# Optimization experiments

Measured on AMD Instinct MI355X. Metric: run time of the kernel, lower is better.

The kernel has to match this reference:

```python
import jax, jax.numpy as jnp
import numpy as np

T, B, C, H = 1024, 4, 1024, 16
NH = C // H  # head_size = 64
E = 32       # TIME_MIX_EXTRA_DIM


def setup_inputs():
    key = jax.random.key(0)
    ks = jax.random.split(key, 12)
    scale = 1.0 / np.sqrt(C)

    def time_p(ratio):
        w = jnp.arange(C, dtype=jnp.float32) / C
        return (1.0 - jnp.power(w, ratio))[None, None, :]

    decay_speed = jnp.array([-6.0 + 5.0 * (h / (C - 1)) ** 0.7 for h in range(C)], jnp.float32)
    tfa = jnp.array([0.1 * ((i + 1) % 3 - 1) for i in range(C)], jnp.float32).reshape(H, NH)
    return dict(
        inputs=jax.random.normal(ks[0], (T, B, C), jnp.float32),
        shifted=jax.random.normal(ks[1], (B, C), jnp.float32),
        state=jnp.zeros((B, H, NH, NH), jnp.float32),
        time_maa_x=time_p(1.0), time_maa_w=time_p(1.0), time_maa_k=time_p(1.0),
        time_maa_v=time_p(1.0), time_maa_r=time_p(0.5), time_maa_g=time_p(0.5),
        time_maa_w1=jax.random.uniform(ks[2], (C, E * 5), jnp.float32, -1e-4, 1e-4),
        time_maa_w2=jax.random.uniform(ks[3], (5, E, C), jnp.float32, -1e-4, 1e-4),
        Wr=jax.random.normal(ks[4], (C, C), jnp.float32) * scale,
        Wk=jax.random.normal(ks[5], (C, C), jnp.float32) * scale,
        Wv=jax.random.normal(ks[6], (C, C), jnp.float32) * scale,
        Wg=jax.random.normal(ks[7], (C, C), jnp.float32) * scale,
        Wo=jax.random.normal(ks[8], (C, C), jnp.float32) * scale,
        time_decay_w1=jax.random.uniform(ks[9], (C, E), jnp.float32, -1e-4, 1e-4),
        time_decay_w2=jax.random.uniform(ks[10], (E, C), jnp.float32, -1e-4, 1e-4),
        time_decay=decay_speed[None, None, :],
        time_faaaa=tfa,
        gn_scale=jnp.ones((C,), jnp.float32) + 0.02 * jax.random.normal(ks[11], (C,), jnp.float32),
        gn_bias=jnp.zeros((C,), jnp.float32),
    )


def _wkv(r, k, v, w, tf, state):
    # r,k,v,w: (T,B,H,N); tf: (H,N,1); state: (B,H,N,N)
    def body(st, inp):
        rt, kt, vt, wt = inp
        a = kt[..., :, None] * vt[..., None, :]              # (B,H,N,N) outer product
        out = jnp.einsum('bhn,bhnm->bhm', rt, tf * a + st)   # (B,H,N)
        st = a + wt[..., None] * st
        return st, out
    state, out = jax.lax.scan(body, state, (r, k, v, w))
    return out, state


def reference(inputs, shifted, state, time_maa_x, time_maa_w, time_maa_k,
              time_maa_v, time_maa_r, time_maa_g, time_maa_w1, time_maa_w2,
              Wr, Wk, Wv, Wg, Wo, time_decay_w1, time_decay_w2, time_decay,
              time_faaaa, gn_scale, gn_bias):
    Tl, Bl, Cl = inputs.shape
    Hh, Nh = time_faaaa.shape
    x = inputs
    prev = jnp.concatenate([shifted[None], inputs[:-1]], axis=0)  # token shift
    xx = prev - x
    new_shifted = inputs[-1]
    xxx = x + xx * time_maa_x
    m = jnp.tanh(xxx.reshape(Tl * Bl, Cl) @ time_maa_w1).reshape(Tl * Bl, 5, -1).transpose(1, 0, 2)
    m = (m @ time_maa_w2).reshape(5, Tl, Bl, Cl)
    mw, mk, mv, mr, mg = m[0], m[1], m[2], m[3], m[4]
    r = (x + xx * (time_maa_r + mr)) @ Wr
    k = (x + xx * (time_maa_k + mk)) @ Wk
    v = (x + xx * (time_maa_v + mv)) @ Wv
    g = jax.nn.swish((x + xx * (time_maa_g + mg)) @ Wg)
    td = jnp.tanh((x + xx * (time_maa_w + mw)) @ time_decay_w1) @ time_decay_w2 + time_decay
    w = jnp.exp(-jnp.exp(td)).reshape(Tl, Bl, Hh, Nh)
    out, new_state = _wkv(r.reshape(Tl, Bl, Hh, Nh), k.reshape(Tl, Bl, Hh, Nh),
                          v.reshape(Tl, Bl, Hh, Nh), w, time_faaaa[:, :, None], state)
    # flax GroupNorm with leading axis as batch: stats over (B, within-group chans)
    xg = out.reshape(Tl, Bl, Hh, Nh)
    mean = xg.mean(axis=(1, 3), keepdims=True)
    var = xg.var(axis=(1, 3), keepdims=True)
    xn = (xg - mean) * jax.lax.rsqrt(var + 1e-5 * 8.0 ** 2)
    out = xn.reshape(Tl, Bl, Cl) * gn_scale + gn_bias
    out = (out * g) @ Wo
    return out, new_shifted, new_state
```

## Files before the change

kernel.cpp:

```cpp
#include <hip/hip_runtime.h>

using uint = unsigned int;
using ushort = unsigned short;
using f32x4 = __attribute__((ext_vector_type(4))) float;
using bf16x8 = __attribute__((ext_vector_type(8))) short;

__device__ __forceinline__ ushort f2bf(float x) {
  uint b = __float_as_uint(x);
  return (ushort)((b + 0x7FFFu + ((b >> 16) & 1u)) >> 16);
}
__device__ __forceinline__ float bf2f(ushort u) { return __uint_as_float(((uint)u) << 16); }

__device__ __forceinline__ void gload16(const void* g, void* l) {
  __builtin_amdgcn_global_load_lds((const __attribute__((address_space(1))) void*)g,
                                   (__attribute__((address_space(3))) void*)l, 16, 0, 0);
}

struct __align__(8) U4 { ushort x, y, z, w; };

__device__ __forceinline__ void convT_impl(const float* src, ushort* oh, ushort* ol, int R, int C, int ldo) {
  const int r0 = blockIdx.x * 32, c0 = blockIdx.y * 32;
  if (r0 >= ldo || c0 >= C) return;
  __shared__ float tile[32][33];
  const int tx = threadIdx.x & 31, ty = threadIdx.x >> 5;
#pragma unroll
  for (int j = 0; j < 4; ++j) {
    const int r = r0 + ty + j * 8;
    tile[ty + j * 8][tx] = (r < R) ? src[(size_t)r * C + c0 + tx] : 0.f;
  }
  __syncthreads();
#pragma unroll
  for (int j = 0; j < 4; ++j) {
    const int c = c0 + ty + j * 8;
    const int r = r0 + tx;
    const float v = tile[tx][ty + j * 8];
    const ushort hb = f2bf(v);
    oh[(size_t)c * ldo + r] = hb;
    if (ol) ol[(size_t)c * ldo + r] = f2bf(v - bf2f(hb));
  }
}

struct ConvBig { const float* s[5]; ushort* oh[5]; ushort* ol[5]; };
__global__ void conv_big_k(ConvBig a) {
  const int z = blockIdx.z;
  convT_impl(a.s[z], a.oh[z], a.ol[z], 1024, 1024, 1024);
}

struct ConvSmall { const float* s[8]; ushort* oh[8]; int R[8]; int C[8]; int ldo[8]; };
__global__ void conv_small_k(ConvSmall a) {
  const int z = blockIdx.z;
  convT_impl(a.s[z], a.oh[z], nullptr, a.R[z], a.C[z], a.ldo[z]);
}

__global__ void mixx_k(const float* __restrict__ x, const float* __restrict__ sh,
                       const float* __restrict__ maa, ushort* __restrict__ xh) {
  const size_t i = ((size_t)blockIdx.x * 256 + threadIdx.x) * 4;
  const size_t row = i >> 10;
  const int col = (int)(i & 1023);
  const float4 xv = *(const float4*)(x + i);
  const float4 pv = (row < 4) ? *(const float4*)(sh + i) : *(const float4*)(x + i - 4096);
  const float4 mv = *(const float4*)(maa + col);
  U4 o;
  o.x = f2bf(xv.x + (pv.x - xv.x) * mv.x);
  o.y = f2bf(xv.y + (pv.y - xv.y) * mv.y);
  o.z = f2bf(xv.z + (pv.z - xv.z) * mv.z);
  o.w = f2bf(xv.w + (pv.w - xv.w) * mv.w);
  *(U4*)(xh + i) = o;
}

struct GemmP {
  const ushort *Ah, *Al, *Bh, *Bl;
  void *out0, *out1;
  const float *aux0, *aux1, *aux2;
  int lda, ldb, M, N, K, epi, split;
};

__device__ __forceinline__ bf16x8 fragld(const ushort* smbase, int byteOff, int rb, int ks, int l) {
  const int row = rb + (l & 15);
  const int kb = (ks << 6) | (((l >> 4) & 3) << 4);
  const int off = byteOff + row * 128 + (kb ^ ((row & 7) << 4));
  return *(const bf16x8*)((const char*)smbase + off);
}

__global__ __launch_bounds__(256, 2) void gemm_k(GemmP p) {
  __shared__ __align__(16) ushort sm[32768];
  const int t = threadIdx.x;
  const int l = t & 63, wid = t >> 6;
  const int wm = wid >> 1, wn = wid & 1;
  const int bm = blockIdx.x, bn = blockIdx.y;

  f32x4 acc[4][4];
#pragma unroll
  for (int i = 0; i < 4; ++i)
#pragma unroll
    for (int j = 0; j < 4; ++j) acc[i][j] = (f32x4){0.f, 0.f, 0.f, 0.f};

  const int srow = t >> 3;
  const int skb = (t & 7) << 4;
  const int KT = (p.K + 63) >> 6;

  for (int kt = 0; kt < KT; ++kt) {
    const int k0 = kt << 6;
    __syncthreads();
#pragma unroll
    for (int j = 0; j < 4; ++j) {
      const int row = srow + j * 32;
      const int srcK = k0 + ((skb ^ ((row & 7) << 4)) >> 1);
      gload16(p.Ah + (size_t)(bm * 128 + row) * p.lda + srcK, (char*)sm + row * 128 + skb);
      gload16(p.Bh + (size_t)(bn * 128 + row) * p.ldb + srcK, (char*)sm + 16384 + row * 128 + skb);
    }
    if (p.split) {
#pragma unroll
      for (int j = 0; j < 4; ++j) {
        const int row = srow + j * 32;
        const int srcK = k0 + ((skb ^ ((row & 7) << 4)) >> 1);
        gload16(p.Al + (size_t)(bm * 128 + row) * p.lda + srcK, (char*)sm + 32768 + row * 128 + skb);
        gload16(p.Bl + (size_t)(bn * 128 + row) * p.ldb + srcK, (char*)sm + 49152 + row * 128 + skb);
      }
    }
    __syncthreads();
#pragma unroll
    for (int ks = 0; ks < 2; ++ks) {
      bf16x8 ah[4], bh[4];
#pragma unroll
      for (int f = 0; f < 4; ++f) {
        ah[f] = fragld(sm, 0, wm * 64 + f * 16, ks, l);
        bh[f] = fragld(sm, 16384, wn * 64 + f * 16, ks, l);
      }
      if (p.split) {
        bf16x8 al[4], bl[4];
#pragma unroll
        for (int f = 0; f < 4; ++f) {
          al[f] = fragld(sm, 32768, wm * 64 + f * 16, ks, l);
          bl[f] = fragld(sm, 49152, wn * 64 + f * 16, ks, l);
        }
#pragma unroll
        for (int mf = 0; mf < 4; ++mf)
#pragma unroll
          for (int nf = 0; nf < 4; ++nf) {
            acc[mf][nf] = __builtin_amdgcn_mfma_f32_16x16x32_bf16(ah[mf], bh[nf], acc[mf][nf], 0, 0, 0);
            acc[mf][nf] = __builtin_amdgcn_mfma_f32_16x16x32_bf16(ah[mf], bl[nf], acc[mf][nf], 0, 0, 0);
            acc[mf][nf] = __builtin_amdgcn_mfma_f32_16x16x32_bf16(al[mf], bh[nf], acc[mf][nf], 0, 0, 0);
          }
      } else {
#pragma unroll
        for (int mf = 0; mf < 4; ++mf)
#pragma unroll
          for (int nf = 0; nf < 4; ++nf)
            acc[mf][nf] = __builtin_amdgcn_mfma_f32_16x16x32_bf16(ah[mf], bh[nf], acc[mf][nf], 0, 0, 0);
      }
    }
  }

  const int rb0 = bm * 128 + wm * 64 + ((l >> 4) << 2);
  const int cb0 = bn * 128 + wn * 64 + (l & 15);
#pragma unroll
  for (int mf = 0; mf < 4; ++mf) {
#pragma unroll
    for (int nf = 0; nf < 4; ++nf) {
      const int col = cb0 + nf * 16;
      if (col >= p.N) continue;
#pragma unroll
      for (int jj = 0; jj < 4; ++jj) {
        const int row = rb0 + mf * 16 + jj;
        const float v = acc[mf][nf][jj];
        const size_t o = (size_t)row * p.N + col;
        if (p.epi == 0) {
          ((float*)p.out0)[o] = v;
        } else if (p.epi == 1) {
          ((ushort*)p.out0)[o] = f2bf(tanhf(v));
        } else if (p.epi == 2) {
          ((float*)p.out0)[o] = v / (1.f + expf(-v));
        } else if (p.epi == 3) {
          const float x = p.aux0[(size_t)row * 1024 + col];
          const float pv = (row < 4) ? p.aux1[(size_t)row * 1024 + col]
                                     : p.aux0[(size_t)(row - 4) * 1024 + col];
          const float xi = x + (pv - x) * (p.aux2[col] + v);
          const ushort hb = f2bf(xi);
          ((ushort*)p.out0)[o] = hb;
          ((ushort*)p.out1)[o] = f2bf(xi - bf2f(hb));
        } else {
          ((float*)p.out0)[o] = expf(-expf(v + p.aux0[col]));
        }
      }
    }
  }
}

__global__ __launch_bounds__(256) void wkv_k(const float* __restrict__ rf, const float* __restrict__ kf,
                                             const float* __restrict__ vf, const float* __restrict__ wf,
                                             const float* __restrict__ tf, const float* __restrict__ st0,
                                             float* __restrict__ so, float* __restrict__ stO) {
  const int bh = blockIdx.x >> 3, mg = blockIdx.x & 7;
  const int wid = threadIdx.x >> 6, l = threadIdx.x & 63;
  const int m = mg * 8 + wid * 2 + (l >> 5);
  const int n = (l & 31) << 1;
  const int b = bh >> 4, h = bh & 15;
  const size_t sOff = ((size_t)bh * 64 + n) * 64 + m;
  float s0 = st0[sOff], s1 = st0[sOff + 64];
  const float u0 = tf[h * 64 + n], u1 = tf[h * 64 + n + 1];
  size_t cur = (size_t)b * 1024 + h * 64;
  float2 r2 = *(const float2*)(rf + cur + n);
  float2 k2 = *(const float2*)(kf + cur + n);
  float2 w2 = *(const float2*)(wf + cur + n);
  float vm = vf[cur + m];
  for (int t = 0; t < 1024; ++t) {
    float2 nr = {0.f, 0.f}, nk = {0.f, 0.f}, nw = {0.f, 0.f};
    float nv = 0.f;
    if (t < 1023) {
      const size_t nx = cur + 4096;
      nr = *(const float2*)(rf + nx + n);
      nk = *(const float2*)(kf + nx + n);
      nw = *(const float2*)(wf + nx + n);
      nv = vf[nx + m];
    }
    const float kv0 = k2.x * vm, kv1 = k2.y * vm;
    float pr = r2.x * fmaf(u0, kv0, s0) + r2.y * fmaf(u1, kv1, s1);
    s0 = fmaf(w2.x, s0, kv0);
    s1 = fmaf(w2.y, s1, kv1);
    pr += __shfl_xor(pr, 1);
    pr += __shfl_xor(pr, 2);
    pr += __shfl_xor(pr, 4);
    pr += __shfl_xor(pr, 8);
    pr += __shfl_xor(pr, 16);
    if ((l & 31) == 0) so[cur + m] = pr;
    cur += 4096;
    r2 = nr; k2 = nk; w2 = nw; vm = nv;
  }
  stO[sOff] = s0;
  stO[sOff + 64] = s1;
}

__global__ __launch_bounds__(256) void gn_k(const float* __restrict__ so, const float* __restrict__ gf,
                                            const float* __restrict__ sc, const float* __restrict__ bi,
                                            ushort* __restrict__ yh, ushort* __restrict__ yl) {
  const int tdx = threadIdx.x;
  const int b = tdx >> 6, n = tdx & 63;
  const int t = blockIdx.x, h = blockIdx.y;
  const size_t idx = (size_t)t * 4096 + (size_t)b * 1024 + h * 64 + n;
  const float v = so[idx];
  float s = v, s2 = v * v;
#pragma unroll
  for (int off = 1; off < 64; off <<= 1) {
    s += __shfl_xor(s, off);
    s2 += __shfl_xor(s2, off);
  }
  __shared__ float ps[4], ps2[4];
  if ((tdx & 63) == 0) { ps[b] = s; ps2[b] = s2; }
  __syncthreads();
  const float S = ps[0] + ps[1] + ps[2] + ps[3];
  const float S2 = ps2[0] + ps2[1] + ps2[2] + ps2[3];
  const float mean = S * (1.f / 256.f);
  const float var = S2 * (1.f / 256.f) - mean * mean;
  const float inv = rsqrtf(var + 6.4e-4f);
  const int c = h * 64 + n;
  float y = (v - mean) * inv * sc[c] + bi[c];
  y *= gf[idx];
  const ushort hb = f2bf(y);
  yh[idx] = hb;
  yl[idx] = f2bf(y - bf2f(hb));
}

extern "C" void kernel_launch(void* const* d_in, const int* in_sizes, int n_in,
                              void* d_out, int out_size, void* d_ws, size_t ws_size,
                              hipStream_t stream) {
  const float* inp = (const float*)d_in[0];
  const float* shifted = (const float*)d_in[1];
  const float* st0 = (const float*)d_in[2];
  const float* maa_x = (const float*)d_in[3];
  const float* maa[5] = {(const float*)d_in[4], (const float*)d_in[5], (const float*)d_in[6],
                         (const float*)d_in[7], (const float*)d_in[8]};
  const float* w1 = (const float*)d_in[9];
  const float* w2 = (const float*)d_in[10];
  const float* W[5] = {(const float*)d_in[11], (const float*)d_in[12], (const float*)d_in[13],
                       (const float*)d_in[14], (const float*)d_in[15]};
  const float* tdw1 = (const float*)d_in[16];
  const float* tdw2 = (const float*)d_in[17];
  const float* tdec = (const float*)d_in[18];
  const float* tf = (const float*)d_in[19];
  const float* gsc = (const float*)d_in[20];
  const float* gbi = (const float*)d_in[21];
  (void)in_sizes; (void)n_in; (void)out_size; (void)ws_size;

  char* ws = (char*)d_ws;
  size_t cur = 0;
  auto alloc = [&](size_t bytes) { char* r = ws + cur; cur += (bytes + 255) & ~(size_t)255; return r; };
  ushort *WT_h[5], *WT_l[5];
  for (int i = 0; i < 5; ++i) {
    WT_h[i] = (ushort*)alloc(1024 * 1024 * 2);
    WT_l[i] = (ushort*)alloc(1024 * 1024 * 2);
  }
  ushort* w1T = (ushort*)alloc(256 * 1024 * 2);
  ushort* tdw1T = (ushort*)alloc(128 * 1024 * 2);
  ushort* tdw2T = (ushort*)alloc(1024 * 64 * 2);
  ushort* w2T = (ushort*)alloc(5 * 1024 * 64 * 2);
  ushort* xxh = (ushort*)alloc(4096ull * 1024 * 2);
  ushort* m1h = (ushort*)alloc(4096ull * 160 * 2 + 256);
  ushort* Xh = (ushort*)alloc(4096ull * 1024 * 2);
  ushort* Xl = (ushort*)alloc(4096ull * 1024 * 2);
  ushort* tdhh = (ushort*)alloc(4096ull * 32 * 2 + 256);
  float* r_f = (float*)alloc(16777216);
  float* k_f = (float*)alloc(16777216);
  float* v_f = (float*)alloc(16777216);
  float* w_f = (float*)alloc(16777216);
  float* g_f = (float*)alloc(16777216);
  float* so_f = (float*)alloc(16777216);
  ushort* yh = (ushort*)alloc(8388608);
  ushort* yl = (ushort*)alloc(8388608);

  ConvBig cb;
  for (int i = 0; i < 5; ++i) { cb.s[i] = W[i]; cb.oh[i] = WT_h[i]; cb.ol[i] = WT_l[i]; }
  conv_big_k<<<dim3(32, 32, 5), 256, 0, stream>>>(cb);
  ConvSmall cs;
  cs.s[0] = w1;   cs.oh[0] = w1T;   cs.R[0] = 1024; cs.C[0] = 160;  cs.ldo[0] = 1024;
  cs.s[1] = tdw1; cs.oh[1] = tdw1T; cs.R[1] = 1024; cs.C[1] = 32;   cs.ldo[1] = 1024;
  cs.s[2] = tdw2; cs.oh[2] = tdw2T; cs.R[2] = 32;   cs.C[2] = 1024; cs.ldo[2] = 64;
  for (int i = 0; i < 5; ++i) {
    cs.s[3 + i] = w2 + (size_t)i * 32 * 1024;
    cs.oh[3 + i] = w2T + (size_t)i * 1024 * 64;
    cs.R[3 + i] = 32; cs.C[3 + i] = 1024; cs.ldo[3 + i] = 64;
  }
  conv_small_k<<<dim3(32, 32, 8), 256, 0, stream>>>(cs);

  mixx_k<<<dim3(4096), 256, 0, stream>>>(inp, shifted, maa_x, xxh);

  auto G = [&](const ushort* Ah, const ushort* Al, int lda, const ushort* Bh, const ushort* Bl, int ldb,
               int N, int K, void* out0, void* out1, int epi, int split,
               const float* a0, const float* a1, const float* a2) {
    GemmP p{Ah, Al, Bh, Bl, out0, out1, a0, a1, a2, lda, ldb, 4096, N, K, epi, split};
    gemm_k<<<dim3(32, (N + 127) / 128), 256, 0, stream>>>(p);
  };

  G(xxh, nullptr, 1024, w1T, nullptr, 1024, 160, 1024, m1h, nullptr, 1, 0, nullptr, nullptr, nullptr);
  G(m1h + 0, nullptr, 160, w2T + 0 * 65536, nullptr, 64, 1024, 32, Xh, Xl, 3, 0, inp, shifted, maa[0]);
  G(Xh, nullptr, 1024, tdw1T, nullptr, 1024, 32, 1024, tdhh, nullptr, 1, 0, nullptr, nullptr, nullptr);
  G(m1h + 96, nullptr, 160, w2T + 3 * 65536, nullptr, 64, 1024, 32, Xh, Xl, 3, 0, inp, shifted, maa[3]);
  G(Xh, Xl, 1024, WT_h[0], WT_l[0], 1024, 1024, 1024, r_f, nullptr, 0, 1, nullptr, nullptr, nullptr);
  G(m1h + 32, nullptr, 160, w2T + 1 * 65536, nullptr, 64, 1024, 32, Xh, Xl, 3, 0, inp, shifted, maa[1]);
  G(Xh, Xl, 1024, WT_h[1], WT_l[1], 1024, 1024, 1024, k_f, nullptr, 0, 1, nullptr, nullptr, nullptr);
  G(m1h + 64, nullptr, 160, w2T + 2 * 65536, nullptr, 64, 1024, 32, Xh, Xl, 3, 0, inp, shifted, maa[2]);
  G(Xh, Xl, 1024, WT_h[2], WT_l[2], 1024, 1024, 1024, v_f, nullptr, 0, 1, nullptr, nullptr, nullptr);
  G(m1h + 128, nullptr, 160, w2T + 4 * 65536, nullptr, 64, 1024, 32, Xh, Xl, 3, 0, inp, shifted, maa[4]);
  G(Xh, Xl, 1024, WT_h[3], WT_l[3], 1024, 1024, 1024, g_f, nullptr, 2, 1, nullptr, nullptr, nullptr);
  G(tdhh, nullptr, 32, tdw2T, nullptr, 64, 1024, 32, w_f, nullptr, 4, 0, tdec, nullptr, nullptr);

  float* stateOut = (float*)d_out + 4194304 + 4096;
  wkv_k<<<dim3(512), 256, 0, stream>>>(r_f, k_f, v_f, w_f, tf, st0, so_f, stateOut);
  gn_k<<<dim3(1024, 16), 256, 0, stream>>>(so_f, g_f, gsc, gbi, yh, yl);
  G(yh, yl, 1024, WT_h[4], WT_l[4], 1024, 1024, 1024, (float*)d_out, nullptr, 0, 1, nullptr, nullptr, nullptr);
  hipMemcpyAsync((float*)d_out + 4194304, inp + 4096ull * 1023, 4096 * sizeof(float),
                 hipMemcpyDeviceToDevice, stream);
}
```

Baseline: 1.049 ms.

## Stage WKV inputs in LDS with double-buffered 32-step async chunks

The recurrent WKV kernel used to load r, k, w and v from global memory one timestep ahead in registers, which left global-memory latency on the serial critical path. It now copies chunks of 32 timesteps into double-buffered shared memory with asynchronous global-to-LDS loads. The next chunk is fetched while the current one is computed, so the inner loop only reads LDS. The block index mapping is also reordered so the 64 batch-head blocks are adjacent. The cost is a block barrier per chunk, more LDS use, and reliance on the barrier waiting for the async loads.

```diff
diff --git a/kernel.cpp b/kernel.cpp
--- a/kernel.cpp
+++ b/kernel.cpp
@@ -14,6 +14,10 @@
 __device__ __forceinline__ void gload16(const void* g, void* l) {
   __builtin_amdgcn_global_load_lds((const __attribute__((address_space(1))) void*)g,
                                    (__attribute__((address_space(3))) void*)l, 16, 0, 0);
+}
+__device__ __forceinline__ void gload4(const void* g, void* l) {
+  __builtin_amdgcn_global_load_lds((const __attribute__((address_space(1))) void*)g,
+                                   (__attribute__((address_space(3))) void*)l, 4, 0, 0);
 }
 
 struct __align__(8) U4 { ushort x, y, z, w; };
@@ -191,41 +195,64 @@
                                              const float* __restrict__ vf, const float* __restrict__ wf,
                                              const float* __restrict__ tf, const float* __restrict__ st0,
                                              float* __restrict__ so, float* __restrict__ stO) {
-  const int bh = blockIdx.x >> 3, mg = blockIdx.x & 7;
-  const int wid = threadIdx.x >> 6, l = threadIdx.x & 63;
-  const int m = mg * 8 + wid * 2 + (l >> 5);
+  __shared__ __align__(16) float sr[2][32][64], sk[2][32][64], sw[2][32][64];
+  __shared__ __align__(16) float sv[2][32][8];
+  const int tl = threadIdx.x;
+  const int l = tl & 63, wid = tl >> 6;
+  const int bh = blockIdx.x & 63;
+  const int mg = blockIdx.x >> 6;
+  const int b = bh >> 4, h = bh & 15;
+  const int ml = wid * 2 + (l >> 5);
+  const int m = mg * 8 + ml;
   const int n = (l & 31) << 1;
-  const int b = bh >> 4, h = bh & 15;
+  const size_t bOff = (size_t)b * 1024 + h * 64;
+
   const size_t sOff = ((size_t)bh * 64 + n) * 64 + m;
   float s0 = st0[sOff], s1 = st0[sOff + 64];
   const float u0 = tf[h * 64 + n], u1 = tf[h * 64 + n + 1];
-  size_t cur = (size_t)b * 1024 + h * 64;
-  float2 r2 = *(const float2*)(rf + cur + n);
-  float2 k2 = *(const float2*)(kf + cur + n);
-  float2 w2 = *(const float2*)(wf + cur + n);
-  float vm = vf[cur + m];
-  for (int t = 0; t < 1024; ++t) {
-    float2 nr = {0.f, 0.f}, nk = {0.f, 0.f}, nw = {0.f, 0.f};
-    float nv = 0.f;
-    if (t < 1023) {
-      const size_t nx = cur + 4096;
-      nr = *(const float2*)(rf + nx + n);
-      nk = *(const float2*)(kf + nx + n);
-      nw = *(const float2*)(wf + nx + n);
-      nv = vf[nx + m];
-    }
-    const float kv0 = k2.x * vm, kv1 = k2.y * vm;
-    float pr = r2.x * fmaf(u0, kv0, s0) + r2.y * fmaf(u1, kv1, s1);
-    s0 = fmaf(w2.x, s0, kv0);
-    s1 = fmaf(w2.y, s1, kv1);
-    pr += __shfl_xor(pr, 1);
-    pr += __shfl_xor(pr, 2);
-    pr += __shfl_xor(pr, 4);
-    pr += __shfl_xor(pr, 8);
-    pr += __shfl_xor(pr, 16);
-    if ((l & 31) == 0) so[cur + m] = pr;
-    cur += 4096;
-    r2 = nr; k2 = nk; w2 = nw; vm = nv;
+
+  const int tloc = tl >> 4;
+  const int n4 = (tl & 15) << 2;
+  const int tv = tl >> 3, mv = tl & 7;
+
+  auto stage = [&](int bufS, int c) {
+    const size_t g0 = (size_t)(c << 5) * 4096 + bOff;
+    const size_t ga = g0 + (size_t)tloc * 4096 + n4;
+    gload16(rf + ga, &sr[bufS][tloc][n4]);
+    gload16(kf + ga, &sk[bufS][tloc][n4]);
+    gload16(wf + ga, &sw[bufS][tloc][n4]);
+    const size_t gb = ga + 16 * 4096;
+    gload16(rf + gb, &sr[bufS][tloc + 16][n4]);
+    gload16(kf + gb, &sk[bufS][tloc + 16][n4]);
+    gload16(wf + gb, &sw[bufS][tloc + 16][n4]);
+    gload4(vf + g0 + (size_t)tv * 4096 + (mg << 3) + mv, &sv[bufS][tv][mv]);
+  };
+
+  stage(0, 0);
+  size_t obase = bOff;
+  int buf = 0;
+  for (int c = 0; c < 32; ++c) {
+    __syncthreads();
+    if (c + 1 < 32) stage(buf ^ 1, c + 1);
+#pragma unroll 4
+    for (int tt = 0; tt < 32; ++tt) {
+      const float2 r2 = *(const float2*)&sr[buf][tt][n];
+      const float2 k2 = *(const float2*)&sk[buf][tt][n];
+      const float2 w2 = *(const float2*)&sw[buf][tt][n];
+      const float vm = sv[buf][tt][ml];
+      const float kv0 = k2.x * vm, kv1 = k2.y * vm;
+      float pr = r2.x * fmaf(u0, kv0, s0) + r2.y * fmaf(u1, kv1, s1);
+      s0 = fmaf(w2.x, s0, kv0);
+      s1 = fmaf(w2.y, s1, kv1);
+      pr += __shfl_xor(pr, 1);
+      pr += __shfl_xor(pr, 2);
+      pr += __shfl_xor(pr, 4);
+      pr += __shfl_xor(pr, 8);
+      pr += __shfl_xor(pr, 16);
+      if ((l & 31) == 0) so[obase + m] = pr;
+      obase += 4096;
+    }
+    buf ^= 1;
   }
   stO[sOff] = s0;
   stO[sOff + 64] = s1;
```

New measurement: 883.2 us. 1.19x faster.
